# Optimization experiments

Hardware: AMD Instinct MI355X
Metric: run time of the kernel (lower is better)

Reference implementation:

```python
import jax, jax.numpy as jnp
import numpy as np

# ---- module constants (from init_kwargs) ----
EMBED_DIM = 384
NUM_HYPEREDGES = 128
TOPK = 64
SPATIAL_SHAPE = (16, 32, 32)  # D, H, W -> N = 16384
SPACING = (2.0, 1.0, 1.0)
SPATIAL_WEIGHT = 0.1
B, N, C = 4, 16 * 32 * 32, EMBED_DIM


def _l2norm(x, axis=-1, eps=1e-12):
    n = jnp.linalg.norm(x, axis=axis, keepdims=True)
    return x / jnp.maximum(n, eps)


def _get_3d_coords():
    D, H, W = SPATIAL_SHAPE
    z = jnp.arange(D, dtype=jnp.float32) * SPACING[0]
    y = jnp.arange(H, dtype=jnp.float32) * SPACING[1]
    x = jnp.arange(W, dtype=jnp.float32) * SPACING[2]
    zz, yy, xx = jnp.meshgrid(z, y, x, indexing='ij')
    return jnp.stack([zz, yy, xx], axis=-1).reshape(-1, 3)  # (N, 3)


def setup_inputs() -> dict:
    key = jax.random.key(0)
    k1, k2 = jax.random.split(key)
    node_features = jax.random.normal(k1, (B, N, C), dtype=jnp.float32)
    class_token = jax.random.normal(k2, (1, 1, C), dtype=jnp.float32)
    temperature = jnp.ones((1,), dtype=jnp.float32) * 0.07
    return {"node_features": node_features, "class_token": class_token, "temperature": temperature}


def reference(node_features, class_token, temperature):
    Ne = NUM_HYPEREDGES
    w = SPATIAL_WEIGHT
    temp = temperature[0]

    nodes_n = _l2norm(node_features)                      # (B, N, C)

    # Step 1: center sampling by semantic similarity to class token
    ct_n = _l2norm(jnp.broadcast_to(class_token, (B, 1, C)))
    scores = jnp.einsum('boc,bnc->bn', ct_n, nodes_n) / temp  # (B, N)
    _, center_idx = jax.lax.top_k(scores, Ne)             # (B, Ne)

    # Gather centers and compute cosine sim of every center vs all nodes
    centers = jnp.take_along_axis(node_features, center_idx[:, :, None], axis=1)  # (B, Ne, C)
    centers_n = _l2norm(centers)
    sem_sim = jnp.einsum('bec,bnc->ben', centers_n, nodes_n) / temp  # (B, Ne, N)

    # Spatial bias (normalized distance from each center voxel)
    coords = _get_3d_coords()                             # (N, 3)
    center_coords = coords[center_idx]                    # (B, Ne, 3)
    diff = coords[None, None, :, :] - center_coords[:, :, None, :]  # (B, Ne, N, 3)
    dist = jnp.linalg.norm(diff, axis=-1)                 # (B, Ne, N)
    dist = dist / (jnp.max(dist, axis=-1, keepdims=True) + 1e-8)
    combined = (1.0 - w) * sem_sim + w * (1.0 - dist)     # (B, Ne, N)

    # Per-hyperedge top-K neighbors -> incidence matrix H (B, N, Ne)
    _, nbr_idx = jax.lax.top_k(combined, TOPK)            # (B, Ne, K)
    b_ix = jnp.arange(B)[:, None, None]
    e_ix = jnp.arange(Ne)[None, :, None]
    Hmat = jnp.zeros((B, N, Ne), dtype=node_features.dtype)
    Hmat = Hmat.at[b_ix, nbr_idx, e_ix].set(1.0)
    return Hmat
```

## Files before the change

### kernel.cpp

```cpp
#include <hip/hip_runtime.h>
#include <math.h>

#define BB 4
#define NN 16384
#define CC 384
#define NE 128
#define KK 64
#define CAP 1024

typedef unsigned short ushort_t;
typedef __attribute__((ext_vector_type(8))) short bf16x8;
typedef __attribute__((ext_vector_type(4))) float f32x4;
#define MFMA(a, b, c) __builtin_amdgcn_mfma_f32_16x16x32_bf16(a, b, c, 0, 0, 0)

__device__ inline unsigned fkey(float f) {
    unsigned b = __float_as_uint(f);
    return (b & 0x80000000u) ? ~b : (b | 0x80000000u);
}
__device__ inline ushort_t bf16rne(float f) {
    unsigned u = __float_as_uint(f);
    unsigned r = u + 0x7FFFu + ((u >> 16) & 1u);
    return (ushort_t)(r >> 16);
}
__device__ inline float bf16tof(ushort_t h) {
    return __uint_as_float(((unsigned)h) << 16);
}
__device__ inline void cvt2(float fa, float fb, unsigned& hp, unsigned& lp) {
    unsigned ua = __float_as_uint(fa), ub = __float_as_uint(fb);
    unsigned ra = ua + 0x8000u, rb = ub + 0x8000u;
    hp = (ra >> 16) | (rb & 0xFFFF0000u);
    float ha = __uint_as_float(ra & 0xFFFF0000u);
    float hb = __uint_as_float(rb & 0xFFFF0000u);
    float la = fa - ha, lb = fb - hb;
    unsigned lra = __float_as_uint(la) + 0x8000u;
    unsigned lrb = __float_as_uint(lb) + 0x8000u;
    lp = (lra >> 16) | (lrb & 0xFFFF0000u);
}

__device__ inline void bin_select4k(const unsigned* hist, int t, int* wsum,
                                    int* sh_bin, int* sh_r, int r) {
    int base = t * 4;
    int c0 = hist[base], c1 = hist[base + 1], c2 = hist[base + 2], c3 = hist[base + 3];
    int csum = c0 + c1 + c2 + c3;
    int lane = t & 63, wid = t >> 6;
    int x = csum;
#pragma unroll
    for (int off = 1; off < 64; off <<= 1) {
        int v = __shfl_down(x, off, 64);
        if (lane + off < 64) x += v;
    }
    if (lane == 0) wsum[wid] = x;
    __syncthreads();
    int after = 0;
    for (int w2 = wid + 1; w2 < 16; ++w2) after += wsum[w2];
    int S = x - csum + after;
    if (S < r && S + c3 >= r) { *sh_bin = base + 3; *sh_r = r - S; }
    S += c3;
    if (S < r && S + c2 >= r) { *sh_bin = base + 2; *sh_r = r - S; }
    S += c2;
    if (S < r && S + c1 >= r) { *sh_bin = base + 1; *sh_r = r - S; }
    S += c1;
    if (S < r && S + c0 >= r) { *sh_bin = base + 0; *sh_r = r - S; }
    __syncthreads();
}

__global__ __launch_bounds__(256) void k_scores(const float* __restrict__ nf,
                                                const float* __restrict__ ct,
                                                unsigned* __restrict__ keys,
                                                float* __restrict__ invn) {
    int wave = threadIdx.x >> 6;
    int lane = threadIdx.x & 63;
    int row  = blockIdx.x * 4 + wave;
    const float* x = nf + (size_t)row * CC;
    float4 a  = ((const float4*)x)[lane];
    float2 c2 = ((const float2*)(x + 256))[lane];
    float4 ta = ((const float4*)ct)[lane];
    float2 tc = ((const float2*)(ct + 256))[lane];
    float ss = a.x*a.x + a.y*a.y + a.z*a.z + a.w*a.w + c2.x*c2.x + c2.y*c2.y;
    float dt = ta.x*a.x + ta.y*a.y + ta.z*a.z + ta.w*a.w + tc.x*c2.x + tc.y*c2.y;
#pragma unroll
    for (int off = 32; off; off >>= 1) {
        ss += __shfl_xor(ss, off, 64);
        dt += __shfl_xor(dt, off, 64);
    }
    if (lane == 0) {
        float inv = 1.0f / fmaxf(sqrtf(ss), 1e-12f);
        invn[row] = inv;
        keys[row] = fkey(dt * inv);
    }
}

__global__ __launch_bounds__(1024) void k_top128(const unsigned* __restrict__ keys,
                                                 int* __restrict__ cidx,
                                                 float* __restrict__ meta) {
    __shared__ unsigned hist[4096];
    __shared__ int wsum[16];
    __shared__ int sh_bin, sh_r;
    __shared__ unsigned cu[NE];
    __shared__ int cil[NE];
    __shared__ unsigned eqk[CAP];
    __shared__ int eqi[CAP];
    __shared__ int cnt_gt, cnt_eq;
    __shared__ int ocid[NE];
    int b = blockIdx.x;
    int t = threadIdx.x;
    const uint4* rowv = (const uint4*)(keys + b * NN);
    if (t == 0) { cnt_gt = 0; cnt_eq = 0; }
    ((uint4*)hist)[t] = make_uint4(0, 0, 0, 0);
    __syncthreads();
    uint4 u0 = rowv[t], u1 = rowv[t + 1024], u2 = rowv[t + 2048], u3 = rowv[t + 3072];
    atomicAdd(&hist[u0.x >> 20], 1u); atomicAdd(&hist[u0.y >> 20], 1u);
    atomicAdd(&hist[u0.z >> 20], 1u); atomicAdd(&hist[u0.w >> 20], 1u);
    atomicAdd(&hist[u1.x >> 20], 1u); atomicAdd(&hist[u1.y >> 20], 1u);
    atomicAdd(&hist[u1.z >> 20], 1u); atomicAdd(&hist[u1.w >> 20], 1u);
    atomicAdd(&hist[u2.x >> 20], 1u); atomicAdd(&hist[u2.y >> 20], 1u);
    atomicAdd(&hist[u2.z >> 20], 1u); atomicAdd(&hist[u2.w >> 20], 1u);
    atomicAdd(&hist[u3.x >> 20], 1u); atomicAdd(&hist[u3.y >> 20], 1u);
    atomicAdd(&hist[u3.z >> 20], 1u); atomicAdd(&hist[u3.w >> 20], 1u);
    __syncthreads();
    bin_select4k(hist, t, wsum, &sh_bin, &sh_r, NE);
    unsigned bin = (unsigned)sh_bin;
    int r = sh_r;
#define EMIT128(uu, nn) { unsigned tb = (uu) >> 20; \
    if (tb > bin) { int p = atomicAdd(&cnt_gt, 1); cu[p] = (uu); cil[p] = (nn); } \
    else if (tb == bin) { int p = atomicAdd(&cnt_eq, 1); if (p < CAP) { eqk[p] = (uu); eqi[p] = (nn); } } }
    EMIT128(u0.x, 4*t+0); EMIT128(u0.y, 4*t+1); EMIT128(u0.z, 4*t+2); EMIT128(u0.w, 4*t+3);
    EMIT128(u1.x, 4096+4*t+0); EMIT128(u1.y, 4096+4*t+1); EMIT128(u1.z, 4096+4*t+2); EMIT128(u1.w, 4096+4*t+3);
    EMIT128(u2.x, 8192+4*t+0); EMIT128(u2.y, 8192+4*t+1); EMIT128(u2.z, 8192+4*t+2); EMIT128(u2.w, 8192+4*t+3);
    EMIT128(u3.x, 12288+4*t+0); EMIT128(u3.y, 12288+4*t+1); EMIT128(u3.z, 12288+4*t+2); EMIT128(u3.w, 12288+4*t+3);
#undef EMIT128
    __syncthreads();
    int ne = cnt_eq < CAP ? cnt_eq : CAP;
    for (int i = t; i < ne; i += 1024) {
        unsigned ki = eqk[i]; int ii = eqi[i], rk = 0;
        for (int j = 0; j < ne; ++j) {
            unsigned kj = eqk[j];
            rk += (kj > ki) || (kj == ki && eqi[j] < ii);
        }
        if (rk < r) { cu[cnt_gt + rk] = ki; cil[cnt_gt + rk] = ii; }
    }
    __syncthreads();
    if (t < NE) {
        unsigned mu = cu[t]; int mi = cil[t], rk = 0;
#pragma unroll 4
        for (int j = 0; j < NE; ++j) {
            unsigned ou = cu[j]; int oi = cil[j];
            rk += (ou > mu) || (ou == mu && oi < mi);
        }
        ocid[rk] = mi;
        cidx[b * NE + rk] = mi;
    }
    __syncthreads();
    if (t < NE) {
        int ci = ocid[t];
        float zc = (float)(ci >> 10) * 2.0f;
        float yc = (float)((ci >> 5) & 31);
        float xc = (float)(ci & 31);
        float mz = fmaxf(zc * zc, (30.f - zc) * (30.f - zc));
        float my = fmaxf(yc * yc, (31.f - yc) * (31.f - yc));
        float mx = fmaxf(xc * xc, (31.f - xc) * (31.f - xc));
        float md = sqrtf(mz + my + mx);
        int be = b * NE + t;
        meta[be * 4 + 0] = zc;
        meta[be * 4 + 1] = yc;
        meta[be * 4 + 2] = xc;
        meta[be * 4 + 3] = 1.0f / (md + 1e-8f);
    }
}

__global__ __launch_bounds__(64) void k_centers(const float* __restrict__ nf,
                                                const float* __restrict__ invn,
                                                const int* __restrict__ cidx,
                                                ushort_t* __restrict__ Ahi,
                                                ushort_t* __restrict__ Alo) {
    int be = blockIdx.x;
    int b  = be >> 7;
    int l  = threadIdx.x;
    int ci = cidx[be];
    float inv = invn[b * NN + ci];
    const float* src = nf + ((size_t)b * NN + ci) * CC;
    float4 a  = ((const float4*)src)[l];
    float2 c2 = ((const float2*)(src + 256))[l];
    a.x *= inv; a.y *= inv; a.z *= inv; a.w *= inv;
    c2.x *= inv; c2.y *= inv;
    ushort4 h4; ushort2 h2;
    h4.x = bf16rne(a.x); h4.y = bf16rne(a.y); h4.z = bf16rne(a.z); h4.w = bf16rne(a.w);
    h2.x = bf16rne(c2.x); h2.y = bf16rne(c2.y);
    ushort4 l4; ushort2 l2;
    l4.x = bf16rne(a.x - bf16tof(h4.x)); l4.y = bf16rne(a.y - bf16tof(h4.y));
    l4.z = bf16rne(a.z - bf16tof(h4.z)); l4.w = bf16rne(a.w - bf16tof(h4.w));
    l2.x = bf16rne(c2.x - bf16tof(h2.x)); l2.y = bf16rne(c2.y - bf16tof(h2.y));
    ushort_t* dh = Ahi + (size_t)be * CC;
    ushort_t* dl = Alo + (size_t)be * CC;
    ((ushort4*)dh)[l] = h4;
    ((ushort2*)(dh + 256))[l] = h2;
    ((ushort4*)dl)[l] = l4;
    ((ushort2*)(dl + 256))[l] = l2;
}

__global__ __launch_bounds__(256, 4) void k_gemm(const float* __restrict__ nf,
                                                 const ushort_t* __restrict__ Ahi,
                                                 const ushort_t* __restrict__ Alo,
                                                 const float* __restrict__ invn,
                                                 const float* __restrict__ meta,
                                                 const float* __restrict__ temp,
                                                 unsigned* __restrict__ outk) {
    __shared__ ushort_t Ah[4][66][8], Al[4][66][8];
    __shared__ ushort_t Bh[4][130][8], Bl[4][130][8];
    __shared__ float ms[64 * 4];
    __shared__ float invs_s[128];
    int b  = blockIdx.y;
    int x  = blockIdx.x;
    int low = x & 15;
    int e0 = (low >> 3) * 64;
    int nt = (x >> 4) * 8 + (low & 7);
    int n0 = nt * 128;
    int t  = threadIdx.x;
    int w = t >> 6, lane = t & 63, quad = lane >> 4, mrow = lane & 15;
    int m0 = (w & 1) * 32, nw0 = (w >> 1) * 64;
    for (int i = t; i < 64 * 4; i += 256) ms[i] = meta[(b * NE + e0) * 4 + i];
    if (t < 128) invs_s[t] = invn[b * NN + n0 + t];
    f32x4 acc[2][4];
#pragma unroll
    for (int i = 0; i < 2; ++i)
#pragma unroll
        for (int j = 0; j < 4; ++j) acc[i][j] = (f32x4)0.f;
    const ushort_t* Abh = Ahi + ((size_t)b * NE + e0) * CC;
    const ushort_t* Abl = Alo + ((size_t)b * NE + e0) * CC;
    const float* Bb = nf + ((size_t)b * NN + n0) * CC;
    int ae = t >> 2, ak8 = t & 3;
    const ushort_t* agh = Abh + (size_t)ae * CC + ak8 * 8;
    const ushort_t* agl = Abl + (size_t)ae * CC + ak8 * 8;
    int bn0 = t >> 2, bk80 = t & 3;
    int bn1 = (t + 256) >> 2, bk81 = (t + 256) & 3;
    const float* bs0 = Bb + (size_t)bn0 * CC + bk80 * 8;
    const float* bs1 = Bb + (size_t)bn1 * CC + bk81 * 8;
    uint4 pAh, pAl;
    float4 pB0a, pB0b, pB1a, pB1b;
    pAh = *(const uint4*)agh;
    pAl = *(const uint4*)agl;
    pB0a = ((const float4*)bs0)[0]; pB0b = ((const float4*)bs0)[1];
    pB1a = ((const float4*)bs1)[0]; pB1b = ((const float4*)bs1)[1];
    for (int kt = 0; kt < CC; kt += 32) {
        __syncthreads();
        *(uint4*)&Ah[ak8][ae][0] = pAh;
        *(uint4*)&Al[ak8][ae][0] = pAl;
        {
            uint4 ph, pl;
            cvt2(pB0a.x, pB0a.y, ph.x, pl.x);
            cvt2(pB0a.z, pB0a.w, ph.y, pl.y);
            cvt2(pB0b.x, pB0b.y, ph.z, pl.z);
            cvt2(pB0b.z, pB0b.w, ph.w, pl.w);
            *(uint4*)&Bh[bk80][bn0][0] = ph;
            *(uint4*)&Bl[bk80][bn0][0] = pl;
            cvt2(pB1a.x, pB1a.y, ph.x, pl.x);
            cvt2(pB1a.z, pB1a.w, ph.y, pl.y);
            cvt2(pB1b.x, pB1b.y, ph.z, pl.z);
            cvt2(pB1b.z, pB1b.w, ph.w, pl.w);
            *(uint4*)&Bh[bk81][bn1][0] = ph;
            *(uint4*)&Bl[bk81][bn1][0] = pl;
        }
        if (kt + 32 < CC) {
            pAh = *(const uint4*)(agh + kt + 32);
            pAl = *(const uint4*)(agl + kt + 32);
            pB0a = ((const float4*)(bs0 + kt + 32))[0]; pB0b = ((const float4*)(bs0 + kt + 32))[1];
            pB1a = ((const float4*)(bs1 + kt + 32))[0]; pB1b = ((const float4*)(bs1 + kt + 32))[1];
        }
        __syncthreads();
        bf16x8 afh[2], afl[2], bfh[4], bfl[4];
#pragma unroll
        for (int i = 0; i < 2; ++i) {
            int m = m0 + i * 16 + mrow;
            afh[i] = *(const bf16x8*)&Ah[quad][m][0];
            afl[i] = *(const bf16x8*)&Al[quad][m][0];
        }
#pragma unroll
        for (int j = 0; j < 4; ++j) {
            int n = nw0 + j * 16 + mrow;
            bfh[j] = *(const bf16x8*)&Bh[quad][n][0];
            bfl[j] = *(const bf16x8*)&Bl[quad][n][0];
        }
#pragma unroll
        for (int i = 0; i < 2; ++i)
#pragma unroll
            for (int j = 0; j < 4; ++j) {
                acc[i][j] = MFMA(afh[i], bfh[j], acc[i][j]);
                acc[i][j] = MFMA(afh[i], bfl[j], acc[i][j]);
                acc[i][j] = MFMA(afl[i], bfh[j], acc[i][j]);
            }
    }
    float scale = 0.9f / temp[0];
#pragma unroll
    for (int j = 0; j < 4; ++j) {
        int nloc = nw0 + j * 16 + mrow;
        int n = n0 + nloc;
        float invnn = invs_s[nloc];
        float zf = (float)(n >> 10) * 2.0f;
        float yf = (float)((n >> 5) & 31);
        float xf = (float)(n & 31);
#pragma unroll
        for (int i = 0; i < 2; ++i) {
#pragma unroll
            for (int r = 0; r < 4; ++r) {
                int el = m0 + i * 16 + quad * 4 + r;
                float zc = ms[el * 4 + 0], yc = ms[el * 4 + 1], xc = ms[el * 4 + 2], ivd = ms[el * 4 + 3];
                float dz = zf - zc, dy = yf - yc, dx = xf - xc;
                float dist = sqrtf(dz * dz + dy * dy + dx * dx);
                float v = scale * invnn * acc[i][j][r] + 0.1f * (1.0f - dist * ivd);
                outk[((size_t)(b * NE + e0 + el)) * NN + n] = fkey(v);
            }
        }
    }
}

__global__ __launch_bounds__(1024) void k_top64(const unsigned* __restrict__ comb,
                                                unsigned* __restrict__ bmg) {
    __shared__ unsigned hist[4096];
    __shared__ unsigned bm[512];
    __shared__ int wsum[16];
    __shared__ int sh_bin, sh_r;
    __shared__ unsigned eqk[CAP];
    __shared__ int eqi[CAP];
    __shared__ int cnt_eq;
    int be = blockIdx.x;
    int t  = threadIdx.x;
    const uint4* rowv = (const uint4*)(comb + (size_t)be * NN);
    if (t == 0) cnt_eq = 0;
    ((uint4*)hist)[t] = make_uint4(0, 0, 0, 0);
    if (t < 128) ((uint4*)bm)[t] = make_uint4(0, 0, 0, 0);
    __syncthreads();
    uint4 u0 = rowv[t], u1 = rowv[t + 1024], u2 = rowv[t + 2048], u3 = rowv[t + 3072];
    atomicAdd(&hist[u0.x >> 20], 1u); atomicAdd(&hist[u0.y >> 20], 1u);
    atomicAdd(&hist[u0.z >> 20], 1u); atomicAdd(&hist[u0.w >> 20], 1u);
    atomicAdd(&hist[u1.x >> 20], 1u); atomicAdd(&hist[u1.y >> 20], 1u);
    atomicAdd(&hist[u1.z >> 20], 1u); atomicAdd(&hist[u1.w >> 20], 1u);
    atomicAdd(&hist[u2.x >> 20], 1u); atomicAdd(&hist[u2.y >> 20], 1u);
    atomicAdd(&hist[u2.z >> 20], 1u); atomicAdd(&hist[u2.w >> 20], 1u);
    atomicAdd(&hist[u3.x >> 20], 1u); atomicAdd(&hist[u3.y >> 20], 1u);
    atomicAdd(&hist[u3.z >> 20], 1u); atomicAdd(&hist[u3.w >> 20], 1u);
    __syncthreads();
    bin_select4k(hist, t, wsum, &sh_bin, &sh_r, KK);
    unsigned bin = (unsigned)sh_bin;
    int r = sh_r;
#define EMIT64(uu, nn) { unsigned tb = (uu) >> 20; \
    if (tb > bin) { atomicOr(&bm[(nn) >> 5], 1u << ((nn) & 31)); } \
    else if (tb == bin) { int p = atomicAdd(&cnt_eq, 1); if (p < CAP) { eqk[p] = (uu); eqi[p] = (nn); } } }
    EMIT64(u0.x, 4*t+0); EMIT64(u0.y, 4*t+1); EMIT64(u0.z, 4*t+2); EMIT64(u0.w, 4*t+3);
    EMIT64(u1.x, 4096+4*t+0); EMIT64(u1.y, 4096+4*t+1); EMIT64(u1.z, 4096+4*t+2); EMIT64(u1.w, 4096+4*t+3);
    EMIT64(u2.x, 8192+4*t+0); EMIT64(u2.y, 8192+4*t+1); EMIT64(u2.z, 8192+4*t+2); EMIT64(u2.w, 8192+4*t+3);
    EMIT64(u3.x, 12288+4*t+0); EMIT64(u3.y, 12288+4*t+1); EMIT64(u3.z, 12288+4*t+2); EMIT64(u3.w, 12288+4*t+3);
#undef EMIT64
    __syncthreads();
    int ne = cnt_eq < CAP ? cnt_eq : CAP;
    for (int i = t; i < ne; i += 1024) {
        unsigned ki = eqk[i]; int ii = eqi[i], rk = 0;
        for (int j = 0; j < ne; ++j) {
            unsigned kj = eqk[j];
            rk += (kj > ki) || (kj == ki && eqi[j] < ii);
        }
        if (rk < r) atomicOr(&bm[ii >> 5], 1u << (ii & 31));
    }
    __syncthreads();
    if (t < 128) ((uint4*)(bmg + (size_t)be * 512))[t] = ((uint4*)bm)[t];
}

__global__ __launch_bounds__(256) void k_expand(const unsigned* __restrict__ bmg,
                                                float* __restrict__ H) {
    __shared__ unsigned wl[256];
    int b  = blockIdx.y;
    int n0 = blockIdx.x * 64;
    int t  = threadIdx.x;
    int w0 = n0 >> 5;
    wl[t] = bmg[((size_t)b * NE + (t >> 1)) * 512 + w0 + (t & 1)];
    __syncthreads();
    float4* dst = (float4*)(H + ((size_t)b * NN + n0) * NE);
#pragma unroll
    for (int i = 0; i < 8; ++i) {
        int flat = t + 256 * i;
        int nl = flat >> 5, f4 = flat & 31;
        int wsel = nl >> 5, bit = nl & 31;
        int e = f4 * 4;
        float4 v;
        v.x = (float)((wl[(e + 0) * 2 + wsel] >> bit) & 1u);
        v.y = (float)((wl[(e + 1) * 2 + wsel] >> bit) & 1u);
        v.z = (float)((wl[(e + 2) * 2 + wsel] >> bit) & 1u);
        v.w = (float)((wl[(e + 3) * 2 + wsel] >> bit) & 1u);
        dst[flat] = v;
    }
}

extern "C" void kernel_launch(void* const* d_in, const int* in_sizes, int n_in,
                              void* d_out, int out_size, void* d_ws, size_t ws_size,
                              hipStream_t stream) {
    const float* nf   = (const float*)d_in[0];
    const float* ct   = (const float*)d_in[1];
    const float* temp = (const float*)d_in[2];
    float* out = (float*)d_out;

    unsigned* keys = (unsigned*)d_ws;
    float* invn    = (float*)(keys + BB * NN);
    float* meta    = invn + BB * NN;
    ushort_t* Ahi  = (ushort_t*)(meta + BB * NE * 4);
    ushort_t* Alo  = Ahi + (size_t)BB * NE * CC;
    int* cidx      = (int*)(Alo + (size_t)BB * NE * CC);
    unsigned* bmg  = (unsigned*)(cidx + BB * NE);

    k_scores <<<BB * NN / 4, 256, 0, stream>>>(nf, ct, keys, invn);
    k_top128 <<<BB, 1024, 0, stream>>>(keys, cidx, meta);
    k_centers<<<BB * NE, 64, 0, stream>>>(nf, invn, cidx, Ahi, Alo);
    k_gemm   <<<dim3(NN / 128 * 2, BB), 256, 0, stream>>>(nf, Ahi, Alo, invn, meta, temp, (unsigned*)out);
    k_top64  <<<BB * NE, 1024, 0, stream>>>((const unsigned*)out, bmg);
    k_expand <<<dim3(NN / 64, BB), 256, 0, stream>>>(bmg, out);
}
```

Measured before the change: 236.6 us.

## Fuse center gather into top128, retile GEMM to full-E blocks, halve top64 threads

Folds the k_centers kernel into k_top128, removing one launch and the cidx buffer. Retiles the GEMM so each block covers all 128 hyperedges against 64 nodes, which means each fp32 node tile is loaded and split into bf16 hi/lo once instead of twice. The A operand is now streamed straight into LDS with global_load_lds. k_top64 moves to 512 threads, each handling 8 vectors and 8 histogram bins. The trade-off is more LDS per GEMM block, fewer blocks in the top128 stage doing the gather serially, and A loads that are no longer prefetched ahead of the compute.

```diff
diff --git a/kernel.cpp b/kernel.cpp
--- a/kernel.cpp
+++ b/kernel.cpp
@@ -35,6 +35,12 @@
     unsigned lra = __float_as_uint(la) + 0x8000u;
     unsigned lrb = __float_as_uint(lb) + 0x8000u;
     lp = (lra >> 16) | (lrb & 0xFFFF0000u);
+}
+
+__device__ inline void load_lds16(const ushort_t* g, ushort_t* l) {
+    __builtin_amdgcn_global_load_lds(
+        (const __attribute__((address_space(1))) unsigned int*)(const void*)g,
+        (__attribute__((address_space(3))) unsigned int*)(void*)l, 16, 0, 0);
 }
 
 __device__ inline void bin_select4k(const unsigned* hist, int t, int* wsum,
@@ -91,8 +97,11 @@
 }
 
 __global__ __launch_bounds__(1024) void k_top128(const unsigned* __restrict__ keys,
-                                                 int* __restrict__ cidx,
-                                                 float* __restrict__ meta) {
+                                                 const float* __restrict__ nf,
+                                                 const float* __restrict__ invn,
+                                                 float* __restrict__ meta,
+                                                 ushort_t* __restrict__ Ahi,
+                                                 ushort_t* __restrict__ Alo) {
     __shared__ unsigned hist[4096];
     __shared__ int wsum[16];
     __shared__ int sh_bin, sh_r;
@@ -148,7 +157,6 @@
             rk += (ou > mu) || (ou == mu && oi < mi);
         }
         ocid[rk] = mi;
-        cidx[b * NE + rk] = mi;
     }
     __syncthreads();
     if (t < NE) {
@@ -166,36 +174,31 @@
         meta[be * 4 + 2] = xc;
         meta[be * 4 + 3] = 1.0f / (md + 1e-8f);
     }
-}
-
-__global__ __launch_bounds__(64) void k_centers(const float* __restrict__ nf,
-                                                const float* __restrict__ invn,
-                                                const int* __restrict__ cidx,
-                                                ushort_t* __restrict__ Ahi,
-                                                ushort_t* __restrict__ Alo) {
-    int be = blockIdx.x;
-    int b  = be >> 7;
-    int l  = threadIdx.x;
-    int ci = cidx[be];
-    float inv = invn[b * NN + ci];
-    const float* src = nf + ((size_t)b * NN + ci) * CC;
-    float4 a  = ((const float4*)src)[l];
-    float2 c2 = ((const float2*)(src + 256))[l];
-    a.x *= inv; a.y *= inv; a.z *= inv; a.w *= inv;
-    c2.x *= inv; c2.y *= inv;
-    ushort4 h4; ushort2 h2;
-    h4.x = bf16rne(a.x); h4.y = bf16rne(a.y); h4.z = bf16rne(a.z); h4.w = bf16rne(a.w);
-    h2.x = bf16rne(c2.x); h2.y = bf16rne(c2.y);
-    ushort4 l4; ushort2 l2;
-    l4.x = bf16rne(a.x - bf16tof(h4.x)); l4.y = bf16rne(a.y - bf16tof(h4.y));
-    l4.z = bf16rne(a.z - bf16tof(h4.z)); l4.w = bf16rne(a.w - bf16tof(h4.w));
-    l2.x = bf16rne(c2.x - bf16tof(h2.x)); l2.y = bf16rne(c2.y - bf16tof(h2.y));
-    ushort_t* dh = Ahi + (size_t)be * CC;
-    ushort_t* dl = Alo + (size_t)be * CC;
-    ((ushort4*)dh)[l] = h4;
-    ((ushort2*)(dh + 256))[l] = h2;
-    ((ushort4*)dl)[l] = l4;
-    ((ushort2*)(dl + 256))[l] = l2;
+    {
+        int wid2 = t >> 6, lane2 = t & 63;
+        for (int e = wid2; e < NE; e += 16) {
+            int ci = ocid[e];
+            float inv = invn[b * NN + ci];
+            const float* src = nf + ((size_t)b * NN + ci) * CC;
+            float4 a  = ((const float4*)src)[lane2];
+            float2 cv = ((const float2*)(src + 256))[lane2];
+            a.x *= inv; a.y *= inv; a.z *= inv; a.w *= inv;
+            cv.x *= inv; cv.y *= inv;
+            ushort4 h4; ushort2 h2;
+            h4.x = bf16rne(a.x); h4.y = bf16rne(a.y); h4.z = bf16rne(a.z); h4.w = bf16rne(a.w);
+            h2.x = bf16rne(cv.x); h2.y = bf16rne(cv.y);
+            ushort4 l4; ushort2 l2;
+            l4.x = bf16rne(a.x - bf16tof(h4.x)); l4.y = bf16rne(a.y - bf16tof(h4.y));
+            l4.z = bf16rne(a.z - bf16tof(h4.z)); l4.w = bf16rne(a.w - bf16tof(h4.w));
+            l2.x = bf16rne(cv.x - bf16tof(h2.x)); l2.y = bf16rne(cv.y - bf16tof(h2.y));
+            ushort_t* dh = Ahi + ((size_t)b * NE + e) * CC;
+            ushort_t* dl = Alo + ((size_t)b * NE + e) * CC;
+            ((ushort4*)dh)[lane2] = h4;
+            ((ushort2*)(dh + 256))[lane2] = h2;
+            ((ushort4*)dl)[lane2] = l4;
+            ((ushort2*)(dl + 256))[lane2] = l2;
+        }
+    }
 }
 
 __global__ __launch_bounds__(256, 4) void k_gemm(const float* __restrict__ nf,
@@ -205,78 +208,67 @@
                                                  const float* __restrict__ meta,
                                                  const float* __restrict__ temp,
                                                  unsigned* __restrict__ outk) {
-    __shared__ ushort_t Ah[4][66][8], Al[4][66][8];
-    __shared__ ushort_t Bh[4][130][8], Bl[4][130][8];
-    __shared__ float ms[64 * 4];
-    __shared__ float invs_s[128];
+    __shared__ ushort_t Ah[4 * 128 * 8], Al[4 * 128 * 8];
+    __shared__ ushort_t Bh[4][66][8], Bl[4][66][8];
+    __shared__ float ms[NE * 4];
+    __shared__ float invs_s[64];
     int b  = blockIdx.y;
-    int x  = blockIdx.x;
-    int low = x & 15;
-    int e0 = (low >> 3) * 64;
-    int nt = (x >> 4) * 8 + (low & 7);
-    int n0 = nt * 128;
+    int n0 = blockIdx.x * 64;
     int t  = threadIdx.x;
     int w = t >> 6, lane = t & 63, quad = lane >> 4, mrow = lane & 15;
-    int m0 = (w & 1) * 32, nw0 = (w >> 1) * 64;
-    for (int i = t; i < 64 * 4; i += 256) ms[i] = meta[(b * NE + e0) * 4 + i];
-    if (t < 128) invs_s[t] = invn[b * NN + n0 + t];
+    for (int i = t; i < NE * 4; i += 256) ms[i] = meta[b * NE * 4 + i];
+    if (t < 64) invs_s[t] = invn[b * NN + n0 + t];
     f32x4 acc[2][4];
 #pragma unroll
     for (int i = 0; i < 2; ++i)
 #pragma unroll
         for (int j = 0; j < 4; ++j) acc[i][j] = (f32x4)0.f;
-    const ushort_t* Abh = Ahi + ((size_t)b * NE + e0) * CC;
-    const ushort_t* Abl = Alo + ((size_t)b * NE + e0) * CC;
-    const float* Bb = nf + ((size_t)b * NN + n0) * CC;
-    int ae = t >> 2, ak8 = t & 3;
-    const ushort_t* agh = Abh + (size_t)ae * CC + ak8 * 8;
-    const ushort_t* agl = Abl + (size_t)ae * CC + ak8 * 8;
-    int bn0 = t >> 2, bk80 = t & 3;
-    int bn1 = (t + 256) >> 2, bk81 = (t + 256) & 3;
-    const float* bs0 = Bb + (size_t)bn0 * CC + bk80 * 8;
-    const float* bs1 = Bb + (size_t)bn1 * CC + bk81 * 8;
-    uint4 pAh, pAl;
-    float4 pB0a, pB0b, pB1a, pB1b;
-    pAh = *(const uint4*)agh;
-    pAl = *(const uint4*)agl;
-    pB0a = ((const float4*)bs0)[0]; pB0b = ((const float4*)bs0)[1];
-    pB1a = ((const float4*)bs1)[0]; pB1b = ((const float4*)bs1)[1];
+    const ushort_t* Abh = Ahi + (size_t)b * NE * CC;
+    const ushort_t* Abl = Alo + (size_t)b * NE * CC;
+    int q64a = w * 2, q64b = w * 2 + 1;
+    int slota = q64a * 64 + lane, slotb = q64b * 64 + lane;
+    const ushort_t* gha = Abh + (size_t)(slota & 127) * CC + (slota >> 7) * 8;
+    const ushort_t* ghb = Abh + (size_t)(slotb & 127) * CC + (slotb >> 7) * 8;
+    const ushort_t* gla = Abl + (size_t)(slota & 127) * CC + (slota >> 7) * 8;
+    const ushort_t* glb = Abl + (size_t)(slotb & 127) * CC + (slotb >> 7) * 8;
+    ushort_t* ldsAha = &Ah[(q64a * 64) * 8];
+    ushort_t* ldsAhb = &Ah[(q64b * 64) * 8];
+    ushort_t* ldsAla = &Al[(q64a * 64) * 8];
+    ushort_t* ldsAlb = &Al[(q64b * 64) * 8];
+    int bn = t >> 2, bk8 = t & 3;
+    const float* bs = nf + ((size_t)b * NN + n0 + bn) * CC + bk8 * 8;
+    float4 pBa = ((const float4*)bs)[0];
+    float4 pBb = ((const float4*)bs)[1];
     for (int kt = 0; kt < CC; kt += 32) {
         __syncthreads();
-        *(uint4*)&Ah[ak8][ae][0] = pAh;
-        *(uint4*)&Al[ak8][ae][0] = pAl;
+        load_lds16(gha + kt, ldsAha);
+        load_lds16(ghb + kt, ldsAhb);
+        load_lds16(gla + kt, ldsAla);
+        load_lds16(glb + kt, ldsAlb);
         {
             uint4 ph, pl;
-            cvt2(pB0a.x, pB0a.y, ph.x, pl.x);
-            cvt2(pB0a.z, pB0a.w, ph.y, pl.y);
-            cvt2(pB0b.x, pB0b.y, ph.z, pl.z);
-            cvt2(pB0b.z, pB0b.w, ph.w, pl.w);
-            *(uint4*)&Bh[bk80][bn0][0] = ph;
-            *(uint4*)&Bl[bk80][bn0][0] = pl;
-            cvt2(pB1a.x, pB1a.y, ph.x, pl.x);
-            cvt2(pB1a.z, pB1a.w, ph.y, pl.y);
-            cvt2(pB1b.x, pB1b.y, ph.z, pl.z);
-            cvt2(pB1b.z, pB1b.w, ph.w, pl.w);
-            *(uint4*)&Bh[bk81][bn1][0] = ph;
-            *(uint4*)&Bl[bk81][bn1][0] = pl;
+            cvt2(pBa.x, pBa.y, ph.x, pl.x);
+            cvt2(pBa.z, pBa.w, ph.y, pl.y);
+            cvt2(pBb.x, pBb.y, ph.z, pl.z);
+            cvt2(pBb.z, pBb.w, ph.w, pl.w);
+            *(uint4*)&Bh[bk8][bn][0] = ph;
+            *(uint4*)&Bl[bk8][bn][0] = pl;
         }
         if (kt + 32 < CC) {
-            pAh = *(const uint4*)(agh + kt + 32);
-            pAl = *(const uint4*)(agl + kt + 32);
-            pB0a = ((const float4*)(bs0 + kt + 32))[0]; pB0b = ((const float4*)(bs0 + kt + 32))[1];
-            pB1a = ((const float4*)(bs1 + kt + 32))[0]; pB1b = ((const float4*)(bs1 + kt + 32))[1];
+            pBa = ((const float4*)(bs + kt + 32))[0];
+            pBb = ((const float4*)(bs + kt + 32))[1];
         }
         __syncthreads();
         bf16x8 afh[2], afl[2], bfh[4], bfl[4];
 #pragma unroll
         for (int i = 0; i < 2; ++i) {
-            int m = m0 + i * 16 + mrow;
-            afh[i] = *(const bf16x8*)&Ah[quad][m][0];
-            afl[i] = *(const bf16x8*)&Al[quad][m][0];
+            int m = w * 32 + i * 16 + mrow;
+            afh[i] = *(const bf16x8*)&Ah[(quad * 128 + m) * 8];
+            afl[i] = *(const bf16x8*)&Al[(quad * 128 + m) * 8];
         }
 #pragma unroll
         for (int j = 0; j < 4; ++j) {
-            int n = nw0 + j * 16 + mrow;
+            int n = j * 16 + mrow;
             bfh[j] = *(const bf16x8*)&Bh[quad][n][0];
             bfl[j] = *(const bf16x8*)&Bl[quad][n][0];
         }
@@ -292,7 +284,7 @@
     float scale = 0.9f / temp[0];
 #pragma unroll
     for (int j = 0; j < 4; ++j) {
-        int nloc = nw0 + j * 16 + mrow;
+        int nloc = j * 16 + mrow;
         int n = n0 + nloc;
         float invnn = invs_s[nloc];
         float zf = (float)(n >> 10) * 2.0f;
@@ -302,22 +294,22 @@
         for (int i = 0; i < 2; ++i) {
 #pragma unroll
             for (int r = 0; r < 4; ++r) {
-                int el = m0 + i * 16 + quad * 4 + r;
+                int el = w * 32 + i * 16 + quad * 4 + r;
                 float zc = ms[el * 4 + 0], yc = ms[el * 4 + 1], xc = ms[el * 4 + 2], ivd = ms[el * 4 + 3];
                 float dz = zf - zc, dy = yf - yc, dx = xf - xc;
                 float dist = sqrtf(dz * dz + dy * dy + dx * dx);
                 float v = scale * invnn * acc[i][j][r] + 0.1f * (1.0f - dist * ivd);
-                outk[((size_t)(b * NE + e0 + el)) * NN + n] = fkey(v);
+                outk[((size_t)(b * NE + el)) * NN + n] = fkey(v);
             }
         }
     }
 }
 
-__global__ __launch_bounds__(1024) void k_top64(const unsigned* __restrict__ comb,
-                                                unsigned* __restrict__ bmg) {
+__global__ __launch_bounds__(512) void k_top64(const unsigned* __restrict__ comb,
+                                               unsigned* __restrict__ bmg) {
     __shared__ unsigned hist[4096];
     __shared__ unsigned bm[512];
-    __shared__ int wsum[16];
+    __shared__ int wsum[8];
     __shared__ int sh_bin, sh_r;
     __shared__ unsigned eqk[CAP];
     __shared__ int eqi[CAP];
@@ -327,32 +319,57 @@
     const uint4* rowv = (const uint4*)(comb + (size_t)be * NN);
     if (t == 0) cnt_eq = 0;
     ((uint4*)hist)[t] = make_uint4(0, 0, 0, 0);
+    ((uint4*)hist)[t + 512] = make_uint4(0, 0, 0, 0);
     if (t < 128) ((uint4*)bm)[t] = make_uint4(0, 0, 0, 0);
     __syncthreads();
-    uint4 u0 = rowv[t], u1 = rowv[t + 1024], u2 = rowv[t + 2048], u3 = rowv[t + 3072];
-    atomicAdd(&hist[u0.x >> 20], 1u); atomicAdd(&hist[u0.y >> 20], 1u);
-    atomicAdd(&hist[u0.z >> 20], 1u); atomicAdd(&hist[u0.w >> 20], 1u);
-    atomicAdd(&hist[u1.x >> 20], 1u); atomicAdd(&hist[u1.y >> 20], 1u);
-    atomicAdd(&hist[u1.z >> 20], 1u); atomicAdd(&hist[u1.w >> 20], 1u);
-    atomicAdd(&hist[u2.x >> 20], 1u); atomicAdd(&hist[u2.y >> 20], 1u);
-    atomicAdd(&hist[u2.z >> 20], 1u); atomicAdd(&hist[u2.w >> 20], 1u);
-    atomicAdd(&hist[u3.x >> 20], 1u); atomicAdd(&hist[u3.y >> 20], 1u);
-    atomicAdd(&hist[u3.z >> 20], 1u); atomicAdd(&hist[u3.w >> 20], 1u);
-    __syncthreads();
-    bin_select4k(hist, t, wsum, &sh_bin, &sh_r, KK);
+    uint4 u[8];
+#pragma unroll
+    for (int i = 0; i < 8; ++i) u[i] = rowv[t + 512 * i];
+#pragma unroll
+    for (int i = 0; i < 8; ++i) {
+        atomicAdd(&hist[u[i].x >> 20], 1u); atomicAdd(&hist[u[i].y >> 20], 1u);
+        atomicAdd(&hist[u[i].z >> 20], 1u); atomicAdd(&hist[u[i].w >> 20], 1u);
+    }
+    __syncthreads();
+    {
+        int base = t * 8;
+        int c[8]; int csum = 0;
+#pragma unroll
+        for (int i = 0; i < 8; ++i) { c[i] = hist[base + i]; csum += c[i]; }
+        int lane = t & 63, wid = t >> 6;
+        int x = csum;
+#pragma unroll
+        for (int off = 1; off < 64; off <<= 1) {
+            int v = __shfl_down(x, off, 64);
+            if (lane + off < 64) x += v;
+        }
+        if (lane == 0) wsum[wid] = x;
+        __syncthreads();
+        int after = 0;
+        for (int w2 = wid + 1; w2 < 8; ++w2) after += wsum[w2];
+        int S = x - csum + after;
+#pragma unroll
+        for (int i = 7; i >= 0; --i) {
+            if (S < KK && S + c[i] >= KK) { sh_bin = base + i; sh_r = KK - S; }
+            S += c[i];
+        }
+        __syncthreads();
+    }
     unsigned bin = (unsigned)sh_bin;
     int r = sh_r;
 #define EMIT64(uu, nn) { unsigned tb = (uu) >> 20; \
     if (tb > bin) { atomicOr(&bm[(nn) >> 5], 1u << ((nn) & 31)); } \
     else if (tb == bin) { int p = atomicAdd(&cnt_eq, 1); if (p < CAP) { eqk[p] = (uu); eqi[p] = (nn); } } }
-    EMIT64(u0.x, 4*t+0); EMIT64(u0.y, 4*t+1); EMIT64(u0.z, 4*t+2); EMIT64(u0.w, 4*t+3);
-    EMIT64(u1.x, 4096+4*t+0); EMIT64(u1.y, 4096+4*t+1); EMIT64(u1.z, 4096+4*t+2); EMIT64(u1.w, 4096+4*t+3);
-    EMIT64(u2.x, 8192+4*t+0); EMIT64(u2.y, 8192+4*t+1); EMIT64(u2.z, 8192+4*t+2); EMIT64(u2.w, 8192+4*t+3);
-    EMIT64(u3.x, 12288+4*t+0); EMIT64(u3.y, 12288+4*t+1); EMIT64(u3.z, 12288+4*t+2); EMIT64(u3.w, 12288+4*t+3);
+#pragma unroll
+    for (int i = 0; i < 8; ++i) {
+        int nb = 4 * (t + 512 * i);
+        EMIT64(u[i].x, nb + 0); EMIT64(u[i].y, nb + 1);
+        EMIT64(u[i].z, nb + 2); EMIT64(u[i].w, nb + 3);
+    }
 #undef EMIT64
     __syncthreads();
     int ne = cnt_eq < CAP ? cnt_eq : CAP;
-    for (int i = t; i < ne; i += 1024) {
+    for (int i = t; i < ne; i += 512) {
         unsigned ki = eqk[i]; int ii = eqi[i], rk = 0;
         for (int j = 0; j < ne; ++j) {
             unsigned kj = eqk[j];
@@ -402,13 +419,11 @@
     float* meta    = invn + BB * NN;
     ushort_t* Ahi  = (ushort_t*)(meta + BB * NE * 4);
     ushort_t* Alo  = Ahi + (size_t)BB * NE * CC;
-    int* cidx      = (int*)(Alo + (size_t)BB * NE * CC);
-    unsigned* bmg  = (unsigned*)(cidx + BB * NE);
+    unsigned* bmg  = (unsigned*)(Alo + (size_t)BB * NE * CC);
 
     k_scores <<<BB * NN / 4, 256, 0, stream>>>(nf, ct, keys, invn);
-    k_top128 <<<BB, 1024, 0, stream>>>(keys, cidx, meta);
-    k_centers<<<BB * NE, 64, 0, stream>>>(nf, invn, cidx, Ahi, Alo);
-    k_gemm   <<<dim3(NN / 128 * 2, BB), 256, 0, stream>>>(nf, Ahi, Alo, invn, meta, temp, (unsigned*)out);
-    k_top64  <<<BB * NE, 1024, 0, stream>>>((const unsigned*)out, bmg);
+    k_top128 <<<BB, 1024, 0, stream>>>(keys, nf, invn, meta, Ahi, Alo);
+    k_gemm   <<<dim3(NN / 64, BB), 256, 0, stream>>>(nf, Ahi, Alo, invn, meta, temp, (unsigned*)out);
+    k_top64  <<<BB * NE, 512, 0, stream>>>((const unsigned*)out, bmg);
     k_expand <<<dim3(NN / 64, BB), 256, 0, stream>>>(bmg, out);
 }
```

New measurement: 244.1 us. 1.03x slower.
